# Kernel tuning notes

Measured on AMD Instinct MI355X. Metric: run time of the kernel, lower is better.

## Reference

```python
import jax, jax.numpy as jnp
import numpy as np

B, S, D_MODEL = 1, 2048, 2048
H, KVH = 16, 4
HD = D_MODEL // H          # 128
N_REP = H // KVH           # 4 (GQA)
WINDOW = 1024              # window_size=(WINDOW-1, 0): self + 1023 past tokens
CLIP = 8.0
THETA = 500000.0
EPS = 1e-6
SCALE = 1.0 / (HD ** 0.5)


def rms_norm(x, w):
    # per-head RMSNorm over last dim (head_dim)
    var = jnp.mean(jnp.square(x), axis=-1, keepdims=True)
    return x * jax.lax.rsqrt(var + EPS) * w


def rope_tables():
    inv_freq = 1.0 / (THETA ** (jnp.arange(0, HD, 2, dtype=jnp.float32) / HD))
    pos = jnp.arange(S, dtype=jnp.float32)
    freqs = pos[:, None] * inv_freq[None, :]          # [S, HD/2]
    emb = jnp.concatenate([freqs, freqs], axis=-1)    # [S, HD]
    return jnp.cos(emb), jnp.sin(emb)


def rotate_half(x):
    x1, x2 = x[..., : HD // 2], x[..., HD // 2 :]
    return jnp.concatenate([-x2, x1], axis=-1)


def apply_rope(x, cos, sin):
    # x: [B, S, h, HD]; cos/sin: [S, HD]
    return x * cos[None, :, None, :] + rotate_half(x) * sin[None, :, None, :]


def setup_inputs() -> dict:
    key = jax.random.key(0)
    ks = jax.random.split(key, 7)
    w = lambda k, shape: jax.random.normal(k, shape, jnp.float32) * 0.02
    return {
        "x": jax.random.normal(ks[0], (B, S, D_MODEL), jnp.float32),
        "w_q": w(ks[1], (D_MODEL, D_MODEL)),
        "w_k": w(ks[2], (KVH * HD, D_MODEL)),
        "w_v": w(ks[3], (KVH * HD, D_MODEL)),
        "w_out": w(ks[4], (D_MODEL, D_MODEL)),
        "q_norm_w": jnp.ones((HD,), jnp.float32),
        "k_norm_w": jnp.ones((HD,), jnp.float32),
        "sinks": jax.random.normal(ks[5], (H,), jnp.float32),
    }


def reference(x, w_q, w_k, w_v, w_out, q_norm_w, k_norm_w, sinks):
    # fused QKV projection + clip
    q = jnp.clip(x @ w_q.T, -CLIP, CLIP).reshape(B, S, H, HD)
    k = jnp.clip(x @ w_k.T, -CLIP, CLIP).reshape(B, S, KVH, HD)
    v = jnp.clip(x @ w_v.T, -CLIP, CLIP).reshape(B, S, KVH, HD)

    # per-head qk RMSNorm, then RoPE
    q = rms_norm(q, q_norm_w)
    k = rms_norm(k, k_norm_w)
    cos, sin = rope_tables()
    q = apply_rope(q, cos, sin)
    k = apply_rope(k, cos, sin)

    # GQA: repeat_interleave kv heads
    k = jnp.repeat(k, N_REP, axis=2)  # [B, S, H, HD]
    v = jnp.repeat(v, N_REP, axis=2)

    # sliding-window causal attention with a learned per-head sink logit
    logits = jnp.einsum("bqhd,bkhd->bhqk", q, k) * SCALE  # [B, H, S, S]
    qi = jnp.arange(S)[:, None]
    ki = jnp.arange(S)[None, :]
    mask = (ki <= qi) & (ki > qi - WINDOW)                # causal + window
    logits = jnp.where(mask[None, None, :, :], logits, -jnp.inf)

    # sink token: always-visible extra logit sinks[h] with zero value vector
    sink_col = jnp.broadcast_to(sinks[None, :, None, None], (B, H, S, 1))
    full = jnp.concatenate([logits, sink_col], axis=-1)   # [B, H, S, S+1]
    probs = jax.nn.softmax(full, axis=-1)

    att = jnp.einsum("bhqk,bkhd->bqhd", probs[..., :S], v)  # sink value is 0
    return att.reshape(B, S, D_MODEL) @ w_out.T
```

## Files before the change

### kernel.cpp

```cpp
#include <hip/hip_runtime.h>
#include <hip/hip_bf16.h>
#include <math.h>

#define S_LEN 2048
#define DMODEL 2048
#define NH 16
#define NKVH 4
#define HDIM 128
#define WINDOW 1024

typedef __bf16 bf16;
typedef __bf16 bf16x8 __attribute__((ext_vector_type(8)));
typedef float floatx4 __attribute__((ext_vector_type(4)));

static __device__ __forceinline__ bf16x8 load_bf8(const bf16* p) {
    return *reinterpret_cast<const bf16x8*>(p);
}

static __device__ __forceinline__ void async16(const bf16* g, bf16* l) {
    __builtin_amdgcn_global_load_lds(
        (const __attribute__((address_space(1))) void*)g,
        (__attribute__((address_space(3))) void*)l, 16, 0, 0);
}

__global__ __launch_bounds__(256) void convert_kernel(
    const float* __restrict__ x, const float* __restrict__ wq,
    const float* __restrict__ wk, const float* __restrict__ wv,
    const float* __restrict__ wo,
    bf16* __restrict__ xb, bf16* __restrict__ wqb, bf16* __restrict__ wkb,
    bf16* __restrict__ wvb, bf16* __restrict__ wob) {
    int i = blockIdx.x * blockDim.x + threadIdx.x;
    const float* src; bf16* dst; int off;
    if      (i < 1048576) { src = x;  dst = xb;  off = i; }
    else if (i < 2097152) { src = wq; dst = wqb; off = i - 1048576; }
    else if (i < 2359296) { src = wk; dst = wkb; off = i - 2097152; }
    else if (i < 2621440) { src = wv; dst = wvb; off = i - 2359296; }
    else if (i < 3670016) { src = wo; dst = wob; off = i - 2621440; }
    else return;
    float4 v = reinterpret_cast<const float4*>(src)[off];
    union { bf16 b[4]; ushort4 u; } t;
    t.b[0] = (bf16)v.x; t.b[1] = (bf16)v.y; t.b[2] = (bf16)v.z; t.b[3] = (bf16)v.w;
    reinterpret_cast<ushort4*>(dst)[off] = t.u;
}

__global__ __launch_bounds__(256) void gemm_qkv_fused(
    const bf16* __restrict__ A, const bf16* __restrict__ B,
    const float* __restrict__ qw, const float* __restrict__ kw,
    bf16* __restrict__ qb, bf16* __restrict__ kb, bf16* __restrict__ vtb) {
    const int K = 2048;
    __shared__ __align__(16) bf16 sA[2][64 * 32];
    __shared__ __align__(16) bf16 sB[2][128 * 32];
    __shared__ float rowss[64][2];
    __shared__ bf16 xnorm[64][128];
    int tid = threadIdx.x;
    int lane = tid & 63, wid = tid >> 6;
    int l15 = lane & 15, quad = lane >> 4;
    int m0 = blockIdx.y * 64, n0 = blockIdx.x * 128;

    int srow = wid * 16 + (lane >> 2);
    int scol = (lane & 3) * 8;
    const bf16* gA  = A + (size_t)(m0 + srow) * K + scol;
    const bf16* gB0 = B + (size_t)(n0 + srow) * K + scol;
    const bf16* gB1 = gB0 + (size_t)64 * K;
    int lOfA = (wid * 16) * 32;
    int lOfB = (wid * 16) * 32;

    floatx4 acc[2][4];
#pragma unroll
    for (int mi = 0; mi < 2; ++mi)
#pragma unroll
        for (int ni = 0; ni < 4; ++ni) acc[mi][ni] = floatx4{0.f, 0.f, 0.f, 0.f};

    int mb = (wid & 1) * 32, nb = (wid >> 1) * 64;

    async16(gA, sA[0] + lOfA);
    async16(gB0, sB[0] + lOfB);
    async16(gB1, sB[0] + 64 * 32 + lOfB);

    int buf = 0;
    for (int k0 = 0; k0 < K; k0 += 32) {
        __syncthreads();
        if (k0 + 32 < K) {
            async16(gA + k0 + 32, sA[buf ^ 1] + lOfA);
            async16(gB0 + k0 + 32, sB[buf ^ 1] + lOfB);
            async16(gB1 + k0 + 32, sB[buf ^ 1] + 64 * 32 + lOfB);
        }
        bf16x8 af[2], bq[4];
#pragma unroll
        for (int i = 0; i < 2; ++i)
            af[i] = load_bf8(sA[buf] + (mb + i * 16 + l15) * 32 + quad * 8);
#pragma unroll
        for (int i = 0; i < 4; ++i)
            bq[i] = load_bf8(sB[buf] + (nb + i * 16 + l15) * 32 + quad * 8);
#pragma unroll
        for (int mi = 0; mi < 2; ++mi)
#pragma unroll
            for (int ni = 0; ni < 4; ++ni)
                acc[mi][ni] = __builtin_amdgcn_mfma_f32_16x16x32_bf16(
                    af[mi], bq[ni], acc[mi][ni], 0, 0, 0);
        buf ^= 1;
    }

#pragma unroll
    for (int mi = 0; mi < 2; ++mi)
#pragma unroll
        for (int ni = 0; ni < 4; ++ni)
#pragma unroll
            for (int r = 0; r < 4; ++r)
                acc[mi][ni][r] = fminf(fmaxf(acc[mi][ni][r], -8.0f), 8.0f);

    if (n0 >= 2560) {
#pragma unroll
        for (int mi = 0; mi < 2; ++mi)
#pragma unroll
            for (int ni = 0; ni < 4; ++ni)
#pragma unroll
                for (int r = 0; r < 4; ++r) {
                    int row = m0 + mb + mi * 16 + quad * 4 + r;
                    int n = n0 + nb + ni * 16 + l15;
                    vtb[(size_t)(n - 2560) * 2048 + row] = (bf16)acc[mi][ni][r];
                }
        return;
    }

#pragma unroll
    for (int mi = 0; mi < 2; ++mi)
#pragma unroll
        for (int r = 0; r < 4; ++r) {
            float s = 0.f;
#pragma unroll
            for (int ni = 0; ni < 4; ++ni) s += acc[mi][ni][r] * acc[mi][ni][r];
#pragma unroll
            for (int o = 1; o < 16; o <<= 1) s += __shfl_xor(s, o, 64);
            if (l15 == 0) rowss[mb + mi * 16 + quad * 4 + r][wid >> 1] = s;
        }
    __syncthreads();

    const float* nw = (n0 < 2048) ? qw : kw;
#pragma unroll
    for (int mi = 0; mi < 2; ++mi)
#pragma unroll
        for (int r = 0; r < 4; ++r) {
            int row = mb + mi * 16 + quad * 4 + r;
            float var = (rowss[row][0] + rowss[row][1]) * (1.0f / 128.0f);
            float rinv = rsqrtf(var + 1e-6f);
#pragma unroll
            for (int ni = 0; ni < 4; ++ni) {
                int col = nb + ni * 16 + l15;
                float xn = acc[mi][ni][r] * rinv * nw[col];
                acc[mi][ni][r] = xn;
                xnorm[row][col] = (bf16)xn;
            }
        }
    __syncthreads();

    float invf[4];
#pragma unroll
    for (int ni = 0; ni < 4; ++ni) {
        int fi = (nb + ni * 16 + l15) & 63;
        invf[ni] = __expf((float)fi * (-13.122363377404328f / 64.0f));
    }
    bool lowhalf = (nb == 0);
#pragma unroll
    for (int mi = 0; mi < 2; ++mi)
#pragma unroll
        for (int r = 0; r < 4; ++r) {
            int row = mb + mi * 16 + quad * 4 + r;
            float pos = (float)(m0 + row);
#pragma unroll
            for (int ni = 0; ni < 4; ++ni) {
                int col = nb + ni * 16 + l15;
                float ang = pos * invf[ni];
                float c = __cosf(ang), sn = __sinf(ang);
                float part = (float)xnorm[row][col ^ 64];
                float rot = lowhalf ? -part : part;
                float o = acc[mi][ni][r] * c + rot * sn;
                int n = n0 + col;
                int s = m0 + row;
                if (n0 < 2048) qb[(size_t)s * 2048 + n] = (bf16)o;
                else           kb[(size_t)s * 512 + (n - 2048)] = (bf16)o;
            }
        }
}

__global__ __launch_bounds__(256) void gemm_out(
    const bf16* __restrict__ A, const bf16* __restrict__ B,
    float* __restrict__ C) {
    const int K = 2048, N = 2048;
    __shared__ __align__(16) bf16 sA[2][64 * 32];
    __shared__ __align__(16) bf16 sB[2][128 * 32];
    int tid = threadIdx.x;
    int lane = tid & 63, wid = tid >> 6;
    int l15 = lane & 15, quad = lane >> 4;
    int m0 = blockIdx.y * 64, n0 = blockIdx.x * 128;

    int srow = wid * 16 + (lane >> 2);
    int scol = (lane & 3) * 8;
    const bf16* gA  = A + (size_t)(m0 + srow) * K + scol;
    const bf16* gB0 = B + (size_t)(n0 + srow) * K + scol;
    const bf16* gB1 = gB0 + (size_t)64 * K;
    int lOfA = (wid * 16) * 32;
    int lOfB = (wid * 16) * 32;

    floatx4 acc[2][4];
#pragma unroll
    for (int mi = 0; mi < 2; ++mi)
#pragma unroll
        for (int ni = 0; ni < 4; ++ni) acc[mi][ni] = floatx4{0.f, 0.f, 0.f, 0.f};

    int mb = (wid & 1) * 32, nb = (wid >> 1) * 64;

    async16(gA, sA[0] + lOfA);
    async16(gB0, sB[0] + lOfB);
    async16(gB1, sB[0] + 64 * 32 + lOfB);

    int buf = 0;
    for (int k0 = 0; k0 < K; k0 += 32) {
        __syncthreads();
        if (k0 + 32 < K) {
            async16(gA + k0 + 32, sA[buf ^ 1] + lOfA);
            async16(gB0 + k0 + 32, sB[buf ^ 1] + lOfB);
            async16(gB1 + k0 + 32, sB[buf ^ 1] + 64 * 32 + lOfB);
        }
        bf16x8 af[2], bq[4];
#pragma unroll
        for (int i = 0; i < 2; ++i)
            af[i] = load_bf8(sA[buf] + (mb + i * 16 + l15) * 32 + quad * 8);
#pragma unroll
        for (int i = 0; i < 4; ++i)
            bq[i] = load_bf8(sB[buf] + (nb + i * 16 + l15) * 32 + quad * 8);
#pragma unroll
        for (int mi = 0; mi < 2; ++mi)
#pragma unroll
            for (int ni = 0; ni < 4; ++ni)
                acc[mi][ni] = __builtin_amdgcn_mfma_f32_16x16x32_bf16(
                    af[mi], bq[ni], acc[mi][ni], 0, 0, 0);
        buf ^= 1;
    }

#pragma unroll
    for (int mi = 0; mi < 2; ++mi)
#pragma unroll
        for (int ni = 0; ni < 4; ++ni)
#pragma unroll
            for (int r = 0; r < 4; ++r) {
                int m = m0 + mb + mi * 16 + quad * 4 + r;
                int n = n0 + nb + ni * 16 + l15;
                C[(size_t)m * N + n] = acc[mi][ni][r];
            }
}

__global__ __launch_bounds__(256) void attn(
    const bf16* __restrict__ qb, const bf16* __restrict__ kb,
    const bf16* __restrict__ vtb, const float* __restrict__ sinks,
    bf16* __restrict__ attb) {
    __shared__ __align__(16) bf16 sK[2][64 * 128];
    __shared__ __align__(16) bf16 sV[2][128 * 64];
    __shared__ __align__(16) bf16 sP[4][16 * 72];
    int tid = threadIdx.x;
    int lane = tid & 63, wid = tid >> 6;
    int l15 = lane & 15, quad = lane >> 4;
    int h = blockIdx.y, kh = h >> 2;
    int bq0 = blockIdx.x * 64;
    int qw0 = bq0 + wid * 16;
    bf16* myp = sP[wid];

    bf16x8 qf[4];
    const bf16* qrow = qb + (size_t)(qw0 + l15) * 2048 + h * 128 + quad * 8;
#pragma unroll
    for (int kc = 0; kc < 4; ++kc) qf[kc] = load_bf8(qrow + kc * 32);

    floatx4 acc[8];
#pragma unroll
    for (int f = 0; f < 8; ++f) acc[f] = floatx4{0.f, 0.f, 0.f, 0.f};
    float lpart[4] = {0.f, 0.f, 0.f, 0.f};
    int qi_base = qw0 + quad * 4;

    int keyit = wid * 4 + (lane >> 4);
    int gcK = (lane & 15) ^ keyit;
    int dimit = wid * 8 + (lane >> 3);
    int gcV = (lane & 7) ^ ((lane >> 3) & 7);

    int tstart = bq0 - 1024; if (tstart < 0) tstart = 0;
    const bf16* kbase = kb + (size_t)kh * 128;
    const bf16* vbase = vtb + (size_t)kh * 128 * 2048;

#pragma unroll
    for (int r = 0; r < 4; ++r) {
        async16(kbase + (size_t)(tstart + r * 16 + keyit) * 512 + gcK * 8,
                sK[0] + (r * 16 + wid * 4) * 128);
        async16(vbase + (size_t)(r * 32 + dimit) * 2048 + tstart + gcV * 8,
                sV[0] + (r * 32 + wid * 8) * 64);
    }

    int buf = 0;
    for (int t = tstart; t <= bq0; t += 64) {
        __syncthreads();
        if (t + 64 <= bq0) {
#pragma unroll
            for (int r = 0; r < 4; ++r) {
                async16(kbase + (size_t)(t + 64 + r * 16 + keyit) * 512 + gcK * 8,
                        sK[buf ^ 1] + (r * 16 + wid * 4) * 128);
                async16(vbase + (size_t)(r * 32 + dimit) * 2048 + t + 64 + gcV * 8,
                        sV[buf ^ 1] + (r * 32 + wid * 8) * 64);
            }
        }
        bool active = !((t + 63 <= qw0 - WINDOW) || (t > qw0 + 15));
        if (active) {
            floatx4 s[4];
#pragma unroll
            for (int g = 0; g < 4; ++g) s[g] = floatx4{0.f, 0.f, 0.f, 0.f};
#pragma unroll
            for (int g = 0; g < 4; ++g) {
                int key = g * 16 + l15;
#pragma unroll
                for (int kc = 0; kc < 4; ++kc) {
                    int ch = (kc * 4 + quad) ^ l15;
                    bf16x8 b = load_bf8(sK[buf] + key * 128 + ch * 8);
                    s[g] = __builtin_amdgcn_mfma_f32_16x16x32_bf16(qf[kc], b, s[g], 0, 0, 0);
                }
            }
#pragma unroll
            for (int r = 0; r < 4; ++r) {
                int qi = qi_base + r;
                int row = (quad * 4 + r) * 72;
#pragma unroll
                for (int g = 0; g < 4; ++g) {
                    int ki = t + g * 16 + l15;
                    float v = s[g][r] * 0.08838834764831845f;
                    bool ok = (ki <= qi) && (ki > qi - WINDOW);
                    float e = ok ? __expf(v) : 0.0f;
                    lpart[r] += e;
                    myp[row + g * 16 + l15] = (bf16)e;
                }
            }
            bf16x8 pa0 = load_bf8(myp + l15 * 72 + quad * 8);
            bf16x8 pa1 = load_bf8(myp + l15 * 72 + 32 + quad * 8);
#pragma unroll
            for (int f = 0; f < 8; ++f) {
                int dim = f * 16 + l15;
                int ch0 = quad ^ (l15 & 7);
                int ch1 = (4 + quad) ^ (l15 & 7);
                bf16x8 vb0 = load_bf8(sV[buf] + dim * 64 + ch0 * 8);
                bf16x8 vb1 = load_bf8(sV[buf] + dim * 64 + ch1 * 8);
                acc[f] = __builtin_amdgcn_mfma_f32_16x16x32_bf16(pa0, vb0, acc[f], 0, 0, 0);
                acc[f] = __builtin_amdgcn_mfma_f32_16x16x32_bf16(pa1, vb1, acc[f], 0, 0, 0);
            }
        }
        buf ^= 1;
    }

    float sk = __expf(sinks[h]);
#pragma unroll
    for (int r = 0; r < 4; ++r) {
        float rs = lpart[r];
#pragma unroll
        for (int o = 1; o < 16; o <<= 1) rs += __shfl_xor(rs, o, 64);
        float inv = 1.0f / (rs + sk);
        int m = qw0 + quad * 4 + r;
#pragma unroll
        for (int f = 0; f < 8; ++f) {
            attb[(size_t)m * 2048 + h * 128 + f * 16 + l15] = (bf16)(acc[f][r] * inv);
        }
    }
}

extern "C" void kernel_launch(void* const* d_in, const int* in_sizes, int n_in,
                              void* d_out, int out_size, void* d_ws, size_t ws_size,
                              hipStream_t stream) {
    const float* x      = (const float*)d_in[0];
    const float* w_q    = (const float*)d_in[1];
    const float* w_k    = (const float*)d_in[2];
    const float* w_v    = (const float*)d_in[3];
    const float* w_out  = (const float*)d_in[4];
    const float* q_norm = (const float*)d_in[5];
    const float* k_norm = (const float*)d_in[6];
    const float* sinks  = (const float*)d_in[7];

    char* ws = (char*)d_ws;
    const size_t MB = 1u << 20;
    bf16* xb   = (bf16*)(ws + 0 * MB);
    bf16* wqb  = (bf16*)(ws + 8 * MB);
    bf16* wkb  = (bf16*)(ws + 16 * MB);
    bf16* wvb  = (bf16*)(ws + 18 * MB);
    bf16* wob  = (bf16*)(ws + 20 * MB);
    bf16* qb   = (bf16*)(ws + 28 * MB);
    bf16* kb   = (bf16*)(ws + 36 * MB);
    bf16* vtb  = (bf16*)(ws + 38 * MB);
    bf16* attb = (bf16*)(ws + 40 * MB);
    bf16* wcomb = wqb;
    float* out = (float*)d_out;

    convert_kernel<<<14336, 256, 0, stream>>>(x, w_q, w_k, w_v, w_out,
                                              xb, wqb, wkb, wvb, wob);
    gemm_qkv_fused<<<dim3(24, 32), 256, 0, stream>>>(xb, wcomb, q_norm, k_norm,
                                                     qb, kb, vtb);
    attn<<<dim3(32, 16), 256, 0, stream>>>(qb, kb, vtb, sinks, attb);
    gemm_out<<<dim3(16, 32), 256, 0, stream>>>(attb, wob, out);
}
```

Baseline: 223.2 us.

## Enlarge GEMM tiles to 128x128x64 with XOR-swizzled LDS and shared body

Both projection GEMMs now use 128x128 output tiles with a K-step of 64 instead of 64x128 with K-step 32. This doubles per-wave MFMA work per LDS load and halves the number of barriers. LDS rows are XOR-swizzled to avoid bank conflicts, and the xnorm scratch reuses the GEMM shared buffer. The grids shrink to 384 and 256 blocks, which risks under-filling the 256 CUs and adds register pressure from 16 accumulators per wave.

Result: faster. 211.6 us (-5.2%).

```diff
diff --git a/kernel.cpp b/kernel.cpp
--- a/kernel.cpp
+++ b/kernel.cpp
@@ -43,66 +43,65 @@
     reinterpret_cast<ushort4*>(dst)[off] = t.u;
 }
 
+#define GEMM_BODY(EXTRA_LDS_DECLS)                                             \
+    __shared__ __align__(16) bf16 smem[4 * 128 * 64];               \
+    EXTRA_LDS_DECLS                                                            \
+    int tid = threadIdx.x;                                                     \
+    int lane = tid & 63, wid = tid >> 6;                                       \
+    int l15 = lane & 15, quad = lane >> 4;                                     \
+    int rlocal = lane >> 3;                                                    \
+    int scol = ((lane & 7) ^ rlocal) * 8;                                      \
+    const bf16* gA = A + (size_t)(m0 + wid * 32 + rlocal) * K + scol;          \
+    const bf16* gB = B + (size_t)(n0 + wid * 32 + rlocal) * K + scol;          \
+    int ldsOf = (wid * 32) * 64;                                               \
+    floatx4 acc[4][4];                                                         \
+    _Pragma("unroll") for (int mi = 0; mi < 4; ++mi)                           \
+        _Pragma("unroll") for (int ni = 0; ni < 4; ++ni)                       \
+            acc[mi][ni] = floatx4{0.f, 0.f, 0.f, 0.f};                         \
+    int mb = (wid & 1) * 64, nb = (wid >> 1) * 64;                             \
+    _Pragma("unroll") for (int j = 0; j < 4; ++j) {                            \
+        async16(gA + (size_t)(j * 8) * K, smem + ldsOf + j * 512);             \
+        async16(gB + (size_t)(j * 8) * K, smem + 16384 + ldsOf + j * 512);     \
+    }                                                                          \
+    int buf = 0;                                                               \
+    for (int k0 = 0; k0 < K; k0 += 64) {                                       \
+        __syncthreads();                                                       \
+        if (k0 + 64 < K) {                                                     \
+            int nof = (buf ^ 1) * 8192;                                        \
+            _Pragma("unroll") for (int j = 0; j < 4; ++j) {                    \
+                async16(gA + (size_t)(j * 8) * K + k0 + 64,                    \
+                        smem + nof + ldsOf + j * 512);                         \
+                async16(gB + (size_t)(j * 8) * K + k0 + 64,                    \
+                        smem + 16384 + nof + ldsOf + j * 512);                 \
+            }                                                                  \
+        }                                                                      \
+        const bf16* sA = smem + buf * 8192;                                    \
+        const bf16* sB = smem + 16384 + buf * 8192;                            \
+        _Pragma("unroll") for (int kc = 0; kc < 2; ++kc) {                     \
+            bf16x8 af[4], bq[4];                                               \
+            _Pragma("unroll") for (int i = 0; i < 4; ++i) {                    \
+                int ch = ((kc << 2) + quad) ^ (l15 & 7);                       \
+                af[i] = load_bf8(sA + (mb + i * 16 + l15) * 64 + ch * 8);      \
+                bq[i] = load_bf8(sB + (nb + i * 16 + l15) * 64 + ch * 8);      \
+            }                                                                  \
+            _Pragma("unroll") for (int mi = 0; mi < 4; ++mi)                   \
+                _Pragma("unroll") for (int ni = 0; ni < 4; ++ni)               \
+                    acc[mi][ni] = __builtin_amdgcn_mfma_f32_16x16x32_bf16(     \
+                        af[mi], bq[ni], acc[mi][ni], 0, 0, 0);                 \
+        }                                                                      \
+        buf ^= 1;                                                              \
+    }
+
 __global__ __launch_bounds__(256) void gemm_qkv_fused(
     const bf16* __restrict__ A, const bf16* __restrict__ B,
     const float* __restrict__ qw, const float* __restrict__ kw,
     bf16* __restrict__ qb, bf16* __restrict__ kb, bf16* __restrict__ vtb) {
     const int K = 2048;
-    __shared__ __align__(16) bf16 sA[2][64 * 32];
-    __shared__ __align__(16) bf16 sB[2][128 * 32];
-    __shared__ float rowss[64][2];
-    __shared__ bf16 xnorm[64][128];
-    int tid = threadIdx.x;
-    int lane = tid & 63, wid = tid >> 6;
-    int l15 = lane & 15, quad = lane >> 4;
-    int m0 = blockIdx.y * 64, n0 = blockIdx.x * 128;
-
-    int srow = wid * 16 + (lane >> 2);
-    int scol = (lane & 3) * 8;
-    const bf16* gA  = A + (size_t)(m0 + srow) * K + scol;
-    const bf16* gB0 = B + (size_t)(n0 + srow) * K + scol;
-    const bf16* gB1 = gB0 + (size_t)64 * K;
-    int lOfA = (wid * 16) * 32;
-    int lOfB = (wid * 16) * 32;
-
-    floatx4 acc[2][4];
-#pragma unroll
-    for (int mi = 0; mi < 2; ++mi)
-#pragma unroll
-        for (int ni = 0; ni < 4; ++ni) acc[mi][ni] = floatx4{0.f, 0.f, 0.f, 0.f};
-
-    int mb = (wid & 1) * 32, nb = (wid >> 1) * 64;
-
-    async16(gA, sA[0] + lOfA);
-    async16(gB0, sB[0] + lOfB);
-    async16(gB1, sB[0] + 64 * 32 + lOfB);
-
-    int buf = 0;
-    for (int k0 = 0; k0 < K; k0 += 32) {
-        __syncthreads();
-        if (k0 + 32 < K) {
-            async16(gA + k0 + 32, sA[buf ^ 1] + lOfA);
-            async16(gB0 + k0 + 32, sB[buf ^ 1] + lOfB);
-            async16(gB1 + k0 + 32, sB[buf ^ 1] + 64 * 32 + lOfB);
-        }
-        bf16x8 af[2], bq[4];
-#pragma unroll
-        for (int i = 0; i < 2; ++i)
-            af[i] = load_bf8(sA[buf] + (mb + i * 16 + l15) * 32 + quad * 8);
-#pragma unroll
-        for (int i = 0; i < 4; ++i)
-            bq[i] = load_bf8(sB[buf] + (nb + i * 16 + l15) * 32 + quad * 8);
-#pragma unroll
-        for (int mi = 0; mi < 2; ++mi)
-#pragma unroll
-            for (int ni = 0; ni < 4; ++ni)
-                acc[mi][ni] = __builtin_amdgcn_mfma_f32_16x16x32_bf16(
-                    af[mi], bq[ni], acc[mi][ni], 0, 0, 0);
-        buf ^= 1;
-    }
-
-#pragma unroll
-    for (int mi = 0; mi < 2; ++mi)
+    int m0 = blockIdx.y * 128, n0 = blockIdx.x * 128;
+    GEMM_BODY(__shared__ float rowss[128][2];)
+
+#pragma unroll
+    for (int mi = 0; mi < 4; ++mi)
 #pragma unroll
         for (int ni = 0; ni < 4; ++ni)
 #pragma unroll
@@ -111,7 +110,7 @@
 
     if (n0 >= 2560) {
 #pragma unroll
-        for (int mi = 0; mi < 2; ++mi)
+        for (int mi = 0; mi < 4; ++mi)
 #pragma unroll
             for (int ni = 0; ni < 4; ++ni)
 #pragma unroll
@@ -123,8 +122,11 @@
         return;
     }
 
-#pragma unroll
-    for (int mi = 0; mi < 2; ++mi)
+    __syncthreads();
+    bf16 (*xnorm)[128] = (bf16(*)[128])(smem + 16384);
+
+#pragma unroll
+    for (int mi = 0; mi < 4; ++mi)
 #pragma unroll
         for (int r = 0; r < 4; ++r) {
             float s = 0.f;
@@ -138,7 +140,7 @@
 
     const float* nw = (n0 < 2048) ? qw : kw;
 #pragma unroll
-    for (int mi = 0; mi < 2; ++mi)
+    for (int mi = 0; mi < 4; ++mi)
 #pragma unroll
         for (int r = 0; r < 4; ++r) {
             int row = mb + mi * 16 + quad * 4 + r;
@@ -162,7 +164,7 @@
     }
     bool lowhalf = (nb == 0);
 #pragma unroll
-    for (int mi = 0; mi < 2; ++mi)
+    for (int mi = 0; mi < 4; ++mi)
 #pragma unroll
         for (int r = 0; r < 4; ++r) {
             int row = mb + mi * 16 + quad * 4 + r;
@@ -187,59 +189,10 @@
     const bf16* __restrict__ A, const bf16* __restrict__ B,
     float* __restrict__ C) {
     const int K = 2048, N = 2048;
-    __shared__ __align__(16) bf16 sA[2][64 * 32];
-    __shared__ __align__(16) bf16 sB[2][128 * 32];
-    int tid = threadIdx.x;
-    int lane = tid & 63, wid = tid >> 6;
-    int l15 = lane & 15, quad = lane >> 4;
-    int m0 = blockIdx.y * 64, n0 = blockIdx.x * 128;
-
-    int srow = wid * 16 + (lane >> 2);
-    int scol = (lane & 3) * 8;
-    const bf16* gA  = A + (size_t)(m0 + srow) * K + scol;
-    const bf16* gB0 = B + (size_t)(n0 + srow) * K + scol;
-    const bf16* gB1 = gB0 + (size_t)64 * K;
-    int lOfA = (wid * 16) * 32;
-    int lOfB = (wid * 16) * 32;
-
-    floatx4 acc[2][4];
-#pragma unroll
-    for (int mi = 0; mi < 2; ++mi)
-#pragma unroll
-        for (int ni = 0; ni < 4; ++ni) acc[mi][ni] = floatx4{0.f, 0.f, 0.f, 0.f};
-
-    int mb = (wid & 1) * 32, nb = (wid >> 1) * 64;
-
-    async16(gA, sA[0] + lOfA);
-    async16(gB0, sB[0] + lOfB);
-    async16(gB1, sB[0] + 64 * 32 + lOfB);
-
-    int buf = 0;
-    for (int k0 = 0; k0 < K; k0 += 32) {
-        __syncthreads();
-        if (k0 + 32 < K) {
-            async16(gA + k0 + 32, sA[buf ^ 1] + lOfA);
-            async16(gB0 + k0 + 32, sB[buf ^ 1] + lOfB);
-            async16(gB1 + k0 + 32, sB[buf ^ 1] + 64 * 32 + lOfB);
-        }
-        bf16x8 af[2], bq[4];
-#pragma unroll
-        for (int i = 0; i < 2; ++i)
-            af[i] = load_bf8(sA[buf] + (mb + i * 16 + l15) * 32 + quad * 8);
-#pragma unroll
-        for (int i = 0; i < 4; ++i)
-            bq[i] = load_bf8(sB[buf] + (nb + i * 16 + l15) * 32 + quad * 8);
-#pragma unroll
-        for (int mi = 0; mi < 2; ++mi)
-#pragma unroll
-            for (int ni = 0; ni < 4; ++ni)
-                acc[mi][ni] = __builtin_amdgcn_mfma_f32_16x16x32_bf16(
-                    af[mi], bq[ni], acc[mi][ni], 0, 0, 0);
-        buf ^= 1;
-    }
-
-#pragma unroll
-    for (int mi = 0; mi < 2; ++mi)
+    int m0 = blockIdx.y * 128, n0 = blockIdx.x * 128;
+    GEMM_BODY()
+#pragma unroll
+    for (int mi = 0; mi < 4; ++mi)
 #pragma unroll
         for (int ni = 0; ni < 4; ++ni)
 #pragma unroll
@@ -393,8 +346,8 @@
 
     convert_kernel<<<14336, 256, 0, stream>>>(x, w_q, w_k, w_v, w_out,
                                               xb, wqb, wkb, wvb, wob);
-    gemm_qkv_fused<<<dim3(24, 32), 256, 0, stream>>>(xb, wcomb, q_norm, k_norm,
+    gemm_qkv_fused<<<dim3(24, 16), 256, 0, stream>>>(xb, wcomb, q_norm, k_norm,
                                                      qb, kb, vtb);
     attn<<<dim3(32, 16), 256, 0, stream>>>(qb, kb, vtb, sinks, attb);
-    gemm_out<<<dim3(16, 32), 256, 0, stream>>>(attb, wob, out);
-}
+    gemm_out<<<dim3(16, 16), 256, 0, stream>>>(attb, wob, out);
+}
```
